# Kernel optimization log

Hardware: AMD Instinct MI355X
Metric: run time of the kernel (lower is better)

The kernel has to match this reference:

```python
import jax, jax.numpy as jnp
import numpy as np

BLOCK_SIZE = 1024
OUTLIER_SIGMA = 3.0
OUT_FEATURES = 11008
IN_FEATURES = 4096
TOKENS = 64


def _quantize_mixed_np(W):
    """Faithful numpy port of quantize_mixed (BLOCK_SIZE divides numel exactly here)."""
    flat = W.astype(np.float32).reshape(-1)
    nb = flat.size // BLOCK_SIZE
    blocks = flat.reshape(nb, BLOCK_SIZE)
    mu = blocks.mean(axis=1, keepdims=True)
    sig = np.maximum(blocks.std(axis=1, ddof=1, keepdims=True), 1e-8)  # torch.std is unbiased
    outlier = np.abs(blocks - mu) > OUTLIER_SIGMA * sig
    abs_max = np.maximum(np.abs(np.where(outlier, 0.0, blocks)).max(axis=1), 1e-8)
    scales = (abs_max / 127.0).astype(np.float16)
    q = np.clip(np.round(blocks / abs_max[:, None] * 127.0), -127, 127).astype(np.int8)
    all_pos = np.arange(nb, dtype=np.int64)[:, None] * BLOCK_SIZE + np.arange(BLOCK_SIZE, dtype=np.int64)[None, :]
    int8_data = q[~outlier]                      # row-major == torch order
    fp16_data = blocks[outlier].astype(np.float16)
    int8_pos = all_pos[~outlier].astype(np.int32)
    fp16_pos = all_pos[outlier].astype(np.int32)
    block_idx = np.nonzero(~outlier)[0].astype(np.int32)  # block index per int8 value
    return int8_data, fp16_data, scales, int8_pos, fp16_pos, block_idx


def setup_inputs() -> dict:
    key = jax.random.key(0)
    k_x, k_b = jax.random.split(key)
    rng = np.random.default_rng(0)
    W = (rng.standard_normal((OUT_FEATURES, IN_FEATURES)) * 0.02).astype(np.float32)
    int8_data, fp16_data, scales, int8_pos, fp16_pos, block_idx = _quantize_mixed_np(W)
    x = jax.random.normal(k_x, (TOKENS, IN_FEATURES), dtype=jnp.float16)
    bias = jax.random.normal(k_b, (OUT_FEATURES,), dtype=jnp.float16) * jnp.float16(0.02)
    return {
        "x": x,
        "int8_data": jnp.asarray(int8_data),
        "fp16_data": jnp.asarray(fp16_data),
        "scales": jnp.asarray(scales),
        "bias": bias,
        "int8_pos": jnp.asarray(int8_pos),
        "fp16_pos": jnp.asarray(fp16_pos),
        "block_idx": jnp.asarray(block_idx),
    }


def reference(x, int8_data, fp16_data, scales, bias, int8_pos, fp16_pos, block_idx):
    out_features = bias.shape[0]
    in_features = x.shape[1]
    numel = out_features * in_features  # divisible by BLOCK_SIZE for these dims
    # dequantize_mixed: scatter fp16 outliers and dequantized int8 values into flat fp16 buffer
    flat = jnp.zeros((numel,), dtype=jnp.float16)
    flat = flat.at[fp16_pos].set(fp16_data)
    flat = flat.at[int8_pos].set(int8_data.astype(jnp.float16) * scales[block_idx])
    W = flat.reshape(out_features, in_features)
    # F.linear(x, W, bias) in fp16
    return jnp.dot(x.astype(jnp.float16), W.T) + bias
```

## Files before the change

### kernel.cpp

```cpp
#include <hip/hip_runtime.h>
#include <hip/hip_fp16.h>

#define TOK  64
#define INF  4096
#define OUTF 11008

typedef __attribute__((ext_vector_type(8))) _Float16 half8;
typedef __attribute__((ext_vector_type(4))) float floatx4;
typedef __attribute__((ext_vector_type(8))) unsigned short ushort8;

__global__ __launch_bounds__(256) void dequant_i8_kernel(
    const int* __restrict__ data, const int* __restrict__ pos,
    const float* __restrict__ scales, _Float16* __restrict__ W, int n) {
  int i = blockIdx.x * 256 + threadIdx.x;
  const int stride = gridDim.x * 256;
  for (; i < n; i += stride) {
    const int p = pos[i];
    W[p] = (_Float16)((float)data[i] * scales[p >> 10]);
  }
}

__global__ __launch_bounds__(256) void scatter_out_kernel(
    const float* __restrict__ vals, const int* __restrict__ pos,
    _Float16* __restrict__ W, int n) {
  const int i = blockIdx.x * 256 + threadIdx.x;
  if (i < n) W[pos[i]] = (_Float16)vals[i];
}

__global__ __launch_bounds__(256) void gemm_kernel(
    const float* __restrict__ x, const _Float16* __restrict__ W,
    const float* __restrict__ bias, float* __restrict__ out) {
  __shared__ __align__(16) _Float16 As[64 * 64];
  __shared__ __align__(16) _Float16 Bs[16 * 64];

  const int tid  = threadIdx.x;
  const int wave = tid >> 6;
  const int lane = tid & 63;
  const int n0   = blockIdx.x * 16;

  floatx4 acc = {0.f, 0.f, 0.f, 0.f};

  const int arow = wave * 16 + (lane & 15);
  const int brow = lane & 15;
  const int koff = (lane >> 4) * 8;

  for (int k0 = 0; k0 < INF; k0 += 64) {
#pragma unroll
    for (int it = 0; it < 2; ++it) {
      const int c = tid + it * 256;
      const int r = c >> 3, cc = (c & 7) * 8;
      const floatx4 f0 = *(const floatx4*)&x[r * INF + k0 + cc];
      const floatx4 f1 = *(const floatx4*)&x[r * INF + k0 + cc + 4];
      half8 h;
      h[0] = (_Float16)f0[0]; h[1] = (_Float16)f0[1];
      h[2] = (_Float16)f0[2]; h[3] = (_Float16)f0[3];
      h[4] = (_Float16)f1[0]; h[5] = (_Float16)f1[1];
      h[6] = (_Float16)f1[2]; h[7] = (_Float16)f1[3];
      *(half8*)&As[r * 64 + cc] = h;
    }
    if (tid < 128) {
      const int r = tid >> 3, cc = (tid & 7) * 8;
      *(ushort8*)&Bs[r * 64 + cc] =
          *(const ushort8*)&W[(n0 + r) * INF + k0 + cc];
    }
    __syncthreads();
#pragma unroll
    for (int kk = 0; kk < 64; kk += 32) {
      half8 a = *(const half8*)&As[arow * 64 + kk + koff];
      half8 b = *(const half8*)&Bs[brow * 64 + kk + koff];
      acc = __builtin_amdgcn_mfma_f32_16x16x32_f16(a, b, acc, 0, 0, 0);
    }
    __syncthreads();
  }

  const int n    = n0 + (lane & 15);
  const int quad = lane >> 4;
  const float bv = bias[n];
#pragma unroll
  for (int i = 0; i < 4; ++i) {
    const int t = wave * 16 + quad * 4 + i;
    out[t * OUTF + n] = acc[i] + bv;
  }
}

extern "C" void kernel_launch(void* const* d_in, const int* in_sizes, int n_in,
                              void* d_out, int out_size, void* d_ws,
                              size_t ws_size, hipStream_t stream) {
  const float* x         = (const float*)d_in[0];
  const int*   int8_data = (const int*)d_in[1];
  const float* fp16_data = (const float*)d_in[2];
  const float* scales    = (const float*)d_in[3];
  const float* bias      = (const float*)d_in[4];
  const int*   int8_pos  = (const int*)d_in[5];
  const int*   fp16_pos  = (const int*)d_in[6];

  _Float16* W   = (_Float16*)d_ws;
  float*    out = (float*)d_out;

  const int n8 = in_sizes[1];
  const int nf = in_sizes[2];

  dequant_i8_kernel<<<4096, 256, 0, stream>>>(int8_data, int8_pos, scales, W, n8);
  scatter_out_kernel<<<(nf + 255) / 256, 256, 0, stream>>>(fp16_data, fp16_pos, W, nf);
  gemm_kernel<<<OUTF / 16, 256, 0, stream>>>(x, W, bias, out);
}
```

Measured before the change: 539.8 us.

## Fuse mixed int8/fp16 dequantization into the GEMM and drop the W buffer

Removes the separate scatter-dequant kernels and the intermediate fp16 weight matrix. Each lane rebuilds its weight fragments on the fly, using the row-major ordering of the int8 and outlier streams plus per-quant-block outlier prefix counts, computed by binary search in a small precompute kernel. That kernel also converts x to fp16 once. The GEMM splits K across waves and reduces the partial sums in LDS. This skips reading int8_pos and the scattered writes and re-reads of W, at the cost of per-lane serial outlier merging and scalar, poorly coalesced int8 loads.

```diff
diff --git a/kernel.cpp b/kernel.cpp
--- a/kernel.cpp
+++ b/kernel.cpp
@@ -1,106 +1,154 @@
 #include <hip/hip_runtime.h>
 #include <hip/hip_fp16.h>
 
-#define TOK  64
-#define INF  4096
-#define OUTF 11008
+#define TOK   64
+#define INF   4096
+#define OUTF  11008
+#define NUMEL (OUTF * INF)
+#define NQB   (NUMEL / 1024)
+#define NBLK  (OUTF / 16)
 
 typedef __attribute__((ext_vector_type(8))) _Float16 half8;
+typedef __attribute__((ext_vector_type(4))) _Float16 half4;
 typedef __attribute__((ext_vector_type(4))) float floatx4;
-typedef __attribute__((ext_vector_type(8))) unsigned short ushort8;
 
-__global__ __launch_bounds__(256) void dequant_i8_kernel(
-    const int* __restrict__ data, const int* __restrict__ pos,
-    const float* __restrict__ scales, _Float16* __restrict__ W, int n) {
-  int i = blockIdx.x * 256 + threadIdx.x;
-  const int stride = gridDim.x * 256;
-  for (; i < n; i += stride) {
-    const int p = pos[i];
-    W[p] = (_Float16)((float)data[i] * scales[p >> 10]);
+__global__ __launch_bounds__(256) void precompute_kernel(
+    const float* __restrict__ x, const int* __restrict__ fppos, int nf,
+    _Float16* __restrict__ x16, int* __restrict__ cum) {
+  const int t = blockIdx.x * 256 + threadIdx.x;
+  if (t < (TOK * INF) / 4) {
+    const floatx4 f = *(const floatx4*)&x[t * 4];
+    half4 h;
+    h[0] = (_Float16)f[0]; h[1] = (_Float16)f[1];
+    h[2] = (_Float16)f[2]; h[3] = (_Float16)f[3];
+    *(half4*)&x16[t * 4] = h;
+  }
+  if (t <= NQB) {
+    const int target = t << 10;
+    int lo = 0, hi = nf;
+    while (lo < hi) {
+      const int mid = (lo + hi) >> 1;
+      if (fppos[mid] < target) lo = mid + 1; else hi = mid;
+    }
+    cum[t] = lo;
   }
 }
 
-__global__ __launch_bounds__(256) void scatter_out_kernel(
-    const float* __restrict__ vals, const int* __restrict__ pos,
-    _Float16* __restrict__ W, int n) {
-  const int i = blockIdx.x * 256 + threadIdx.x;
-  if (i < n) W[pos[i]] = (_Float16)vals[i];
-}
-
-__global__ __launch_bounds__(256) void gemm_kernel(
-    const float* __restrict__ x, const _Float16* __restrict__ W,
-    const float* __restrict__ bias, float* __restrict__ out) {
-  __shared__ __align__(16) _Float16 As[64 * 64];
-  __shared__ __align__(16) _Float16 Bs[16 * 64];
+__global__ __launch_bounds__(256) void fused_gemm_kernel(
+    const _Float16* __restrict__ x16, const int* __restrict__ i8,
+    const float* __restrict__ fpdat, const int* __restrict__ fppos,
+    const float* __restrict__ scales, const float* __restrict__ bias,
+    const int* __restrict__ cum, float* __restrict__ out, int n8, int nf) {
+  __shared__ float red[4 * 64 * 16];
 
   const int tid  = threadIdx.x;
   const int wave = tid >> 6;
   const int lane = tid & 63;
+  const int quad = lane >> 4;
+  const int ln   = lane & 15;
   const int n0   = blockIdx.x * 16;
 
-  floatx4 acc = {0.f, 0.f, 0.f, 0.f};
+  const int r = n0 + ln;
+  const int b = r * 4 + wave;
+  const int base = cum[b];
+  const int nxt  = cum[b + 1];
+  const float s  = scales[b];
+  const int n8m1 = n8 - 1;
 
-  const int arow = wave * 16 + (lane & 15);
-  const int brow = lane & 15;
-  const int koff = (lane >> 4) * 8;
+  int j  = base;
+  int qv = (j < nxt) ? fppos[j] : 0x7fffffff;
+  float fv = (j < nxt) ? fpdat[j] : 0.f;
+  int lt = 0;
 
-  for (int k0 = 0; k0 < INF; k0 += 64) {
+  floatx4 acc0 = {0,0,0,0}, acc1 = {0,0,0,0}, acc2 = {0,0,0,0}, acc3 = {0,0,0,0};
+  float ov[8];
 #pragma unroll
-    for (int it = 0; it < 2; ++it) {
-      const int c = tid + it * 256;
-      const int r = c >> 3, cc = (c & 7) * 8;
-      const floatx4 f0 = *(const floatx4*)&x[r * INF + k0 + cc];
-      const floatx4 f1 = *(const floatx4*)&x[r * INF + k0 + cc + 4];
-      half8 h;
-      h[0] = (_Float16)f0[0]; h[1] = (_Float16)f0[1];
-      h[2] = (_Float16)f0[2]; h[3] = (_Float16)f0[3];
-      h[4] = (_Float16)f1[0]; h[5] = (_Float16)f1[1];
-      h[6] = (_Float16)f1[2]; h[7] = (_Float16)f1[3];
-      *(half8*)&As[r * 64 + cc] = h;
+  for (int e = 0; e < 8; ++e) ov[e] = 0.f;
+
+  const int kbase = wave * 1024 + quad * 8;
+
+  for (int st = 0; st < 32; ++st) {
+    const int k = kbase + st * 32;
+    const int p = r * INF + k;
+
+    int f = 0;
+    while (qv < p + 8) {
+      if (qv < p) {
+        ++lt;
+      } else {
+        const int d = qv - p;
+        f |= (1 << d);
+#pragma unroll
+        for (int e = 0; e < 8; ++e) ov[e] = (d == e) ? fv : ov[e];
+      }
+      ++j;
+      qv = (j < nxt) ? fppos[j] : 0x7fffffff;
+      fv = (j < nxt) ? fpdat[j] : 0.f;
     }
-    if (tid < 128) {
-      const int r = tid >> 3, cc = (tid & 7) * 8;
-      *(ushort8*)&Bs[r * 64 + cc] =
-          *(const ushort8*)&W[(n0 + r) * INF + k0 + cc];
+
+    const int i0 = p - base - lt;
+    half8 bh;
+    int c = 0;
+#pragma unroll
+    for (int e = 0; e < 8; ++e) {
+      int ie = i0 + e - c;
+      if (ie > n8m1) ie = n8m1;
+      const float vq = (float)i8[ie] * s;
+      const int flg = (f >> e) & 1;
+      bh[e] = (_Float16)(flg ? ov[e] : vq);
+      c += flg;
     }
-    __syncthreads();
-#pragma unroll
-    for (int kk = 0; kk < 64; kk += 32) {
-      half8 a = *(const half8*)&As[arow * 64 + kk + koff];
-      half8 b = *(const half8*)&Bs[brow * 64 + kk + koff];
-      acc = __builtin_amdgcn_mfma_f32_16x16x32_f16(a, b, acc, 0, 0, 0);
-    }
-    __syncthreads();
+    lt += c;
+
+    const half8 a0 = *(const half8*)&x16[(0 * 16 + ln) * INF + k];
+    const half8 a1 = *(const half8*)&x16[(1 * 16 + ln) * INF + k];
+    const half8 a2 = *(const half8*)&x16[(2 * 16 + ln) * INF + k];
+    const half8 a3 = *(const half8*)&x16[(3 * 16 + ln) * INF + k];
+    acc0 = __builtin_amdgcn_mfma_f32_16x16x32_f16(a0, bh, acc0, 0, 0, 0);
+    acc1 = __builtin_amdgcn_mfma_f32_16x16x32_f16(a1, bh, acc1, 0, 0, 0);
+    acc2 = __builtin_amdgcn_mfma_f32_16x16x32_f16(a2, bh, acc2, 0, 0, 0);
+    acc3 = __builtin_amdgcn_mfma_f32_16x16x32_f16(a3, bh, acc3, 0, 0, 0);
   }
 
-  const int n    = n0 + (lane & 15);
-  const int quad = lane >> 4;
-  const float bv = bias[n];
+  const int mb = quad * 4;
 #pragma unroll
-  for (int i = 0; i < 4; ++i) {
-    const int t = wave * 16 + quad * 4 + i;
-    out[t * OUTF + n] = acc[i] + bv;
+  for (int i = 0; i < 4; ++i) red[wave * 1024 + (0 * 16 + mb + i) * 16 + ln] = acc0[i];
+#pragma unroll
+  for (int i = 0; i < 4; ++i) red[wave * 1024 + (1 * 16 + mb + i) * 16 + ln] = acc1[i];
+#pragma unroll
+  for (int i = 0; i < 4; ++i) red[wave * 1024 + (2 * 16 + mb + i) * 16 + ln] = acc2[i];
+#pragma unroll
+  for (int i = 0; i < 4; ++i) red[wave * 1024 + (3 * 16 + mb + i) * 16 + ln] = acc3[i];
+  __syncthreads();
+
+#pragma unroll
+  for (int c2 = 0; c2 < 4; ++c2) {
+    const int cell = tid + c2 * 256;
+    const int m = cell >> 4, n = cell & 15;
+    const float v = red[cell] + red[1024 + cell] + red[2048 + cell] +
+                    red[3072 + cell] + bias[n0 + n];
+    out[m * OUTF + n0 + n] = v;
   }
 }
 
 extern "C" void kernel_launch(void* const* d_in, const int* in_sizes, int n_in,
                               void* d_out, int out_size, void* d_ws,
                               size_t ws_size, hipStream_t stream) {
-  const float* x         = (const float*)d_in[0];
-  const int*   int8_data = (const int*)d_in[1];
-  const float* fp16_data = (const float*)d_in[2];
-  const float* scales    = (const float*)d_in[3];
-  const float* bias      = (const float*)d_in[4];
-  const int*   int8_pos  = (const int*)d_in[5];
-  const int*   fp16_pos  = (const int*)d_in[6];
+  const float* x      = (const float*)d_in[0];
+  const int*   i8     = (const int*)d_in[1];
+  const float* fpdat  = (const float*)d_in[2];
+  const float* scales = (const float*)d_in[3];
+  const float* bias   = (const float*)d_in[4];
+  const int*   fppos  = (const int*)d_in[6];
 
-  _Float16* W   = (_Float16*)d_ws;
+  _Float16* x16 = (_Float16*)d_ws;
+  int*      cum = (int*)((char*)d_ws + (size_t)TOK * INF * sizeof(_Float16));
   float*    out = (float*)d_out;
 
+  const int nf = in_sizes[2];
   const int n8 = in_sizes[1];
-  const int nf = in_sizes[2];
 
-  dequant_i8_kernel<<<4096, 256, 0, stream>>>(int8_data, int8_pos, scales, W, n8);
-  scatter_out_kernel<<<(nf + 255) / 256, 256, 0, stream>>>(fp16_data, fp16_pos, W, nf);
-  gemm_kernel<<<OUTF / 16, 256, 0, stream>>>(x, W, bias, out);
+  precompute_kernel<<<256, 256, 0, stream>>>(x, fppos, nf, x16, cum);
+  fused_gemm_kernel<<<NBLK, 256, 0, stream>>>(x16, i8, fpdat, fppos, scales,
+                                              bias, cum, out, n8, nf);
 }
```

Result: slower. 554.2 us (+2.7%).
